# Performance work log

Hardware: AMD Instinct MI355X
Metric: run time of the kernel (lower is better)

## Reference

```python
import jax, jax.numpy as jnp
import numpy as np

EMBED_DIM = 512
N_HEADS = 8
HEAD_DIM = EMBED_DIM // N_HEADS
MAX_H = 64
MAX_W = 48
B, H, W = 2, 64, 48


def setup_inputs() -> dict:
    key = jax.random.key(0)
    k1, k2, k3, k4, k5 = jax.random.split(key, 5)
    x = jax.random.normal(k1, (B, H, W, EMBED_DIM), dtype=jnp.float32)
    # Linear weights stored as [in, out] (torch stores [out, in]; math is x @ W_in_out)
    w_qkv = jax.random.normal(k2, (EMBED_DIM, 3 * EMBED_DIM), dtype=jnp.float32) * (EMBED_DIM ** -0.5)
    w_out = jax.random.normal(k3, (EMBED_DIM, EMBED_DIM), dtype=jnp.float32) * (EMBED_DIM ** -0.5)
    rel_row_tab = jax.random.normal(k4, (2 * MAX_H - 1, N_HEADS), dtype=jnp.float32) * 0.02
    rel_col_tab = jax.random.normal(k5, (2 * MAX_W - 1, N_HEADS), dtype=jnp.float32) * 0.02
    return {"x": x, "w_qkv": w_qkv, "w_out": w_out,
            "rel_row_tab": rel_row_tab, "rel_col_tab": rel_col_tab}


def _rel_bias(rel_row_tab, rel_col_tab, height, width):
    # 2D relative position bias: [n_heads, S, S]
    row_idx = jnp.repeat(jnp.arange(height), width)          # [S]
    col_idx = jnp.tile(jnp.arange(width), height)            # [S]
    rel_row = jnp.clip(row_idx[:, None] - row_idx[None, :] + MAX_H - 1, 0, 2 * MAX_H - 2)
    rel_col = jnp.clip(col_idx[:, None] - col_idx[None, :] + MAX_W - 1, 0, 2 * MAX_W - 2)
    bias = rel_row_tab[rel_row] + rel_col_tab[rel_col]       # [S, S, n_heads]
    return jnp.transpose(bias, (2, 0, 1))                    # [n_heads, S, S]


def reference(x, w_qkv, w_out, rel_row_tab, rel_col_tab):
    b, h, w, d = x.shape
    s = h * w
    x_flat = x.reshape(b, s, d)
    qkv = x_flat @ w_qkv                                     # [b, s, 3d]
    qkv = qkv.reshape(b, s, 3, N_HEADS, HEAD_DIM)
    qkv = jnp.transpose(qkv, (2, 0, 3, 1, 4))                # [3, b, nh, s, hd]
    q, k, v = qkv[0], qkv[1], qkv[2]
    scale = HEAD_DIM ** -0.5
    attn = jnp.einsum('bhqd,bhkd->bhqk', q, k) * scale       # [b, nh, s, s]
    attn = attn + _rel_bias(rel_row_tab, rel_col_tab, h, w)[None]
    attn = jax.nn.softmax(attn, axis=-1)
    out = jnp.einsum('bhqk,bhkd->bhqd', attn, v)             # [b, nh, s, hd]
    out = jnp.transpose(out, (0, 2, 1, 3)).reshape(b, s, d)
    out = out @ w_out
    return out.reshape(b, h, w, d)
```

## Files before the change

### kernel.cpp

```cpp
#include <hip/hip_runtime.h>
#include <hip/hip_bf16.h>

#define S_TOK 3072
#define NHEADS 8

typedef __attribute__((ext_vector_type(8))) short short8;
typedef __attribute__((ext_vector_type(4))) float floatx4;
typedef __attribute__((ext_vector_type(4))) unsigned short ushortx4;

__device__ __forceinline__ unsigned short f2bf(float f) {
  union { float f; unsigned u; } v; v.f = f;
  unsigned r = v.u + 0x7fffu + ((v.u >> 16) & 1u);
  return (unsigned short)(r >> 16);
}
__device__ __forceinline__ float bf2f(unsigned short h) {
  union { unsigned u; float f; } v; v.u = (unsigned)h << 16;
  return v.f;
}
__device__ __forceinline__ unsigned pack2bf(float a, float b) {
  __hip_bfloat162 h = __float22bfloat162_rn(make_float2(a, b));
  union { __hip_bfloat162 h; unsigned u; } c; c.h = h;
  return c.u;
}
__device__ __forceinline__ void gload16(const void* g, void* l) {
  __builtin_amdgcn_global_load_lds(
      (const __attribute__((address_space(1))) unsigned int*)g,
      (__attribute__((address_space(3))) unsigned int*)l, 16, 0, 0);
}

__global__ __launch_bounds__(256) void ga_conv_x(
    const float* __restrict__ X, unsigned short* __restrict__ xh,
    unsigned short* __restrict__ xl) {
  const int c = blockIdx.x * 256 + threadIdx.x;
  const int m = c >> 6;
  const int c8 = (c & 63) << 3;
  const float* src = X + (size_t)m * 512 + c8;
  float4 v0 = *(const float4*)src, v1 = *(const float4*)(src + 4);
  float vv[8] = {v0.x, v0.y, v0.z, v0.w, v1.x, v1.y, v1.z, v1.w};
  union { unsigned short s[8]; short8 v; } hh, ll;
#pragma unroll
  for (int e = 0; e < 8; ++e) {
    hh.s[e] = f2bf(vv[e]);
    ll.s[e] = f2bf(vv[e] - bf2f(hh.s[e]));
  }
  const size_t dst = (size_t)m * 512 + (c8 ^ ((m & 7) << 3));
  *(short8*)&xh[dst] = hh.v;
  *(short8*)&xl[dst] = ll.v;
}

__global__ __launch_bounds__(256) void ga_conv_wt(
    const float* __restrict__ W, unsigned short* __restrict__ th,
    unsigned short* __restrict__ tl, int N) {
  const int k0 = blockIdx.x * 64, n0 = blockIdx.y * 64;
  const int t = threadIdx.x;
  __shared__ float Ts[64][65];
#pragma unroll
  for (int i = 0; i < 4; ++i) {
    const int r = (t >> 4) + i * 16, c4 = (t & 15) * 4;
    float4 v = *(const float4*)&W[(size_t)(k0 + r) * N + n0 + c4];
    Ts[r][c4] = v.x; Ts[r][c4 + 1] = v.y; Ts[r][c4 + 2] = v.z; Ts[r][c4 + 3] = v.w;
  }
  __syncthreads();
#pragma unroll
  for (int j = 0; j < 2; ++j) {
    const int chunk = t * 2 + j;
    const int nl = chunk >> 3, m8 = chunk & 7;
    const int n = n0 + nl;
    const int ks = (m8 * 8) ^ ((n & 7) << 3);
    union { unsigned short s[8]; short8 v; } hh, ll;
#pragma unroll
    for (int e = 0; e < 8; ++e) {
      float f = Ts[ks + e][nl];
      hh.s[e] = f2bf(f);
      ll.s[e] = f2bf(f - bf2f(hh.s[e]));
    }
    const size_t dst = (size_t)n * 512 + k0 + m8 * 8;
    *(short8*)&th[dst] = hh.v;
    *(short8*)&tl[dst] = ll.v;
  }
}

template <int BM, int BN, int WHICH>
__global__ __launch_bounds__(256, 2) void ga_mm3(
    const unsigned short* __restrict__ Ah, const unsigned short* __restrict__ Al,
    const unsigned short* __restrict__ Bh, const unsigned short* __restrict__ Bl,
    unsigned short* __restrict__ Qd, unsigned short* __restrict__ Kd,
    unsigned short* __restrict__ Vd, float* __restrict__ Out) {
  const int tid = threadIdx.x;
  const int w = tid >> 6, l = tid & 63;
  const int g = l >> 4, ln = l & 15;
  const int wm = w >> 1, wn = w & 1;
  const int m0 = blockIdx.x * BM;
  const int n0 = blockIdx.y * BN;
  constexpr int MI = BM / 32;
  constexpr int NI = BN / 32;
  __shared__ unsigned short Alds[2][BM * 64];
  __shared__ unsigned short Blds[2][BN * 64];
  floatx4 acc[MI][NI];
#pragma unroll
  for (int mi = 0; mi < MI; ++mi)
#pragma unroll
    for (int ni = 0; ni < NI; ++ni)
#pragma unroll
      for (int r = 0; r < 4; ++r) acc[mi][ni][r] = 0.f;

  for (int k0 = 0; k0 < 512; k0 += 64) {
    __syncthreads();
    {
      constexpr int PWA = (BM * 128) / 4096;
      constexpr int PWB = (BN * 128) / 4096;
      const char* ga_h = (const char*)(Ah + (size_t)m0 * 512 + k0);
      const char* ga_l = (const char*)(Al + (size_t)m0 * 512 + k0);
      const char* gb_h = (const char*)(Bh + (size_t)n0 * 512 + k0);
      const char* gb_l = (const char*)(Bl + (size_t)n0 * 512 + k0);
#pragma unroll
      for (int i = 0; i < PWA; ++i) {
        const int off = (w * PWA + i) * 1024;
        const int gb = ((off >> 7) + (l >> 3)) * 1024 + (l & 7) * 16;
        gload16(ga_h + gb, (char*)&Alds[0][0] + off);
        gload16(ga_l + gb, (char*)&Alds[1][0] + off);
      }
#pragma unroll
      for (int i = 0; i < PWB; ++i) {
        const int off = (w * PWB + i) * 1024;
        const int gb = ((off >> 7) + (l >> 3)) * 1024 + (l & 7) * 16;
        gload16(gb_h + gb, (char*)&Blds[0][0] + off);
        gload16(gb_l + gb, (char*)&Blds[1][0] + off);
      }
    }
    asm volatile("s_waitcnt vmcnt(0)" ::: "memory");
    __syncthreads();
#pragma unroll
    for (int kk = 0; kk < 64; kk += 32) {
      const int kbase = kk + g * 8;
      short8 ah[MI], al[MI], bh[NI], bl[NI];
#pragma unroll
      for (int mi = 0; mi < MI; ++mi) {
        const int row = wm * (BM / 2) + mi * 16 + ln;
        const int a = row * 64 + (kbase ^ ((row & 7) << 3));
        ah[mi] = *(const short8*)&Alds[0][a];
        al[mi] = *(const short8*)&Alds[1][a];
      }
#pragma unroll
      for (int ni = 0; ni < NI; ++ni) {
        const int row = wn * (BN / 2) + ni * 16 + ln;
        const int a = row * 64 + (kbase ^ ((row & 7) << 3));
        bh[ni] = *(const short8*)&Blds[0][a];
        bl[ni] = *(const short8*)&Blds[1][a];
      }
#pragma unroll
      for (int mi = 0; mi < MI; ++mi)
#pragma unroll
        for (int ni = 0; ni < NI; ++ni) {
          acc[mi][ni] = __builtin_amdgcn_mfma_f32_16x16x32_bf16(
              ah[mi], bh[ni], acc[mi][ni], 0, 0, 0);
          acc[mi][ni] = __builtin_amdgcn_mfma_f32_16x16x32_bf16(
              al[mi], bh[ni], acc[mi][ni], 0, 0, 0);
          acc[mi][ni] = __builtin_amdgcn_mfma_f32_16x16x32_bf16(
              ah[mi], bl[ni], acc[mi][ni], 0, 0, 0);
        }
    }
  }
  if constexpr (WHICH == 0) {
    const int b = m0 / S_TOK;
    const int s_base = (m0 % S_TOK) + wm * (BM / 2);
#pragma unroll
    for (int ni = 0; ni < NI; ++ni) {
      const int ng = n0 + wn * (BN / 2) + ni * 16;
      const int which = ng >> 9;
      const int h = (ng >> 6) & 7;
      const int d = (ng & 63) + ln;
      unsigned short* hp = (which == 0 ? Qd : which == 1 ? Kd : Vd) +
                           (size_t)(b * 8 + h) * S_TOK * 64;
      const float qs = (which == 0) ? 0.18033688f : 1.0f;
#pragma unroll
      for (int mi = 0; mi < MI; ++mi)
#pragma unroll
        for (int r = 0; r < 4; ++r) {
          const int s = s_base + mi * 16 + g * 4 + r;
          const size_t idx =
              (size_t)s * 64 + ((which == 1) ? (d ^ ((s & 7) << 3)) : d);
          hp[idx] = f2bf(acc[mi][ni][r] * qs);
        }
    }
  } else {
#pragma unroll
    for (int mi = 0; mi < MI; ++mi)
#pragma unroll
      for (int ni = 0; ni < NI; ++ni)
#pragma unroll
        for (int r = 0; r < 4; ++r)
          Out[(size_t)(m0 + wm * (BM / 2) + mi * 16 + g * 4 + r) * 512 + n0 +
              wn * (BN / 2) + ni * 16 + ln] = acc[mi][ni][r];
  }
}

__global__ __launch_bounds__(256) void ga_vtrans(
    const unsigned short* __restrict__ V, unsigned short* __restrict__ Vt2) {
  const int t = threadIdx.x;
  const int tile = blockIdx.x;
  const int bh = blockIdx.y;
  __shared__ unsigned short Ts[96][72];
  const unsigned short* vp = V + ((size_t)bh * S_TOK + tile * 96) * 64;
#pragma unroll
  for (int it = 0; it < 3; ++it) {
    int c = it * 256 + t;
    int s = c >> 3, d8 = c & 7;
    short8 v = *(const short8*)&vp[(size_t)s * 64 + d8 * 8];
    *(short8*)&Ts[s][d8 * 8] = v;
  }
  __syncthreads();
  unsigned short* op = Vt2 + ((size_t)bh * 32 + tile) * 8192;
#pragma unroll
  for (int it = 0; it < 4; ++it) {
    int c2 = it * 256 + t;
    int a = c2 * 8;
    int d = a >> 7;
    int pos0 = (a & 127) ^ ((d & 7) << 3);
    short8 o;
    if (pos0 < 96) {
      const int base = (pos0 & 96) + ((pos0 >> 3) & 3) * 4;
#pragma unroll
      for (int j = 0; j < 8; ++j) {
        const int key = base + ((j >> 2) << 4) + (j & 3);
        o[j] = (short)Ts[key][d];
      }
    } else {
#pragma unroll
      for (int j = 0; j < 8; ++j) o[j] = 0;
    }
    *(short8*)&op[a] = o;
  }
}

__global__ __launch_bounds__(256) void ga_attn16(
    const unsigned short* __restrict__ Q, const unsigned short* __restrict__ Kg,
    const unsigned short* __restrict__ Vt2, const float* __restrict__ rowtab,
    const float* __restrict__ coltab, float* __restrict__ Opart,
    float* __restrict__ Lpart, int tiles_per_split) {
  const int tid = threadIdx.x;
  const int w = tid >> 6;
  const int l = tid & 63;
  const int g = l >> 4;
  const int ln = l & 15;
  const int bh = blockIdx.y;
  const int sp = blockIdx.z;
  const int h = bh & 7;
  const int q0 = blockIdx.x * 128 + w * 32;

  __shared__ float rtab[127];
  __shared__ float ctab[95];
  __shared__ unsigned short Klds[6144];
  __shared__ unsigned short Vlds[8192];
  for (int i = tid; i < 127; i += 256) rtab[i] = rowtab[i * 8 + h] * 1.44269504f;
  for (int i = tid; i < 95; i += 256) ctab[i] = coltab[i * 8 + h] * 1.44269504f;
  __syncthreads();

  const unsigned short* Qp = Q + (size_t)bh * S_TOK * 64;
  const unsigned short* Kp = Kg + (size_t)bh * S_TOK * 64;
  const unsigned short* Vp = Vt2 + (size_t)bh * 32 * 8192;

  int qr[2], qc[2];
  short8 qf[2][2];
  float ctr[2][3][4];
#pragma unroll
  for (int u = 0; u < 2; ++u) {
    const int q = q0 + u * 16 + ln;
    qr[u] = q / 48;
    qc[u] = q - qr[u] * 48;
    qf[u][0] = *(const short8*)&Qp[(size_t)q * 64 + g * 8];
    qf[u][1] = *(const short8*)&Qp[(size_t)q * 64 + 32 + g * 8];
    const float* cb = &ctab[qc[u] - g * 4 + 47];
#pragma unroll
    for (int m = 0; m < 3; ++m)
#pragma unroll
      for (int r = 0; r < 4; ++r) ctr[u][m][r] = cb[-(16 * m + r)];
  }

  short8 ones;
  {
    union { unsigned short s[8]; short8 v; } on;
#pragma unroll
    for (int j = 0; j < 8; ++j) on.s[j] = 0x3F80;
    ones = on.v;
  }

  floatx4 o_acc[2][4];
  floatx4 o5[2];
#pragma unroll
  for (int u = 0; u < 2; ++u) {
#pragma unroll
    for (int r = 0; r < 4; ++r) o5[u][r] = 0.f;
#pragma unroll
    for (int dt = 0; dt < 4; ++dt)
#pragma unroll
      for (int r = 0; r < 4; ++r) o_acc[u][dt][r] = 0.f;
  }

  const int t0 = sp * tiles_per_split;
  for (int t = t0; t < t0 + tiles_per_split; ++t) {
    __syncthreads();
    {
      const char* kg = (const char*)(Kp + (size_t)t * 96 * 64);
      const char* vg = (const char*)(Vp + (size_t)t * 8192);
#pragma unroll
      for (int i = 0; i < 3; ++i) {
        const int off = w * 3072 + i * 1024;
        gload16(kg + off + l * 16, (char*)Klds + off);
      }
#pragma unroll
      for (int i = 0; i < 4; ++i) {
        const int off = w * 4096 + i * 1024;
        gload16(vg + off + l * 16, (char*)Vlds + off);
      }
      asm volatile("s_waitcnt vmcnt(0)" ::: "memory");
      __syncthreads();
    }
    float rt[2][2];
#pragma unroll
    for (int u = 0; u < 2; ++u) {
      rt[u][0] = rtab[qr[u] + 63 - 2 * t] - 12.0f;
      rt[u][1] = rtab[qr[u] + 62 - 2 * t] - 12.0f;
    }
    const int swz = (ln & 7) << 3;
#pragma unroll
    for (int kc32 = 0; kc32 < 3; ++kc32) {
      float e[2][2][4];
#pragma unroll
      for (int kh = 0; kh < 2; ++kh) {
        const int kt = kc32 * 2 + kh;
        const int rb = (kt * 16 + ln) * 64;
        short8 kf0 = *(const short8*)&Klds[rb + ((g * 8) ^ swz)];
        short8 kf1 = *(const short8*)&Klds[rb + ((32 + g * 8) ^ swz)];
        const int m = kt % 3, wrap = kt / 3;
#pragma unroll
        for (int u = 0; u < 2; ++u) {
          floatx4 s = {0.f, 0.f, 0.f, 0.f};
          s = __builtin_amdgcn_mfma_f32_16x16x32_bf16(kf0, qf[u][0], s, 0, 0, 0);
          s = __builtin_amdgcn_mfma_f32_16x16x32_bf16(kf1, qf[u][1], s, 0, 0, 0);
          const float rtw = rt[u][wrap];
#pragma unroll
          for (int r = 0; r < 4; ++r)
            e[u][kh][r] = __builtin_amdgcn_exp2f(s[r] + rtw + ctr[u][m][r]);
        }
      }
      short8 pf[2];
#pragma unroll
      for (int u = 0; u < 2; ++u) {
        union { unsigned uu[4]; short8 v; } pk;
        pk.uu[0] = pack2bf(e[u][0][0], e[u][0][1]);
        pk.uu[1] = pack2bf(e[u][0][2], e[u][0][3]);
        pk.uu[2] = pack2bf(e[u][1][0], e[u][1][1]);
        pk.uu[3] = pack2bf(e[u][1][2], e[u][1][3]);
        pf[u] = pk.v;
      }
#pragma unroll
      for (int dt = 0; dt < 4; ++dt) {
        const int vrow = dt * 16 + ln;
        short8 vf = *(const short8*)&Vlds[vrow * 128 +
                                          ((kc32 * 32 + g * 8) ^ swz)];
        o_acc[0][dt] =
            __builtin_amdgcn_mfma_f32_16x16x32_bf16(pf[0], vf, o_acc[0][dt], 0, 0, 0);
        o_acc[1][dt] =
            __builtin_amdgcn_mfma_f32_16x16x32_bf16(pf[1], vf, o_acc[1][dt], 0, 0, 0);
      }
      o5[0] = __builtin_amdgcn_mfma_f32_16x16x32_bf16(pf[0], ones, o5[0], 0, 0, 0);
      o5[1] = __builtin_amdgcn_mfma_f32_16x16x32_bf16(pf[1], ones, o5[1], 0, 0, 0);
    }
  }
  const size_t rowbase = (size_t)(sp * 16 + bh) * S_TOK;
#pragma unroll
  for (int u = 0; u < 2; ++u) {
    if (ln == 0) {
#pragma unroll
      for (int r = 0; r < 4; ++r)
        Lpart[rowbase + q0 + u * 16 + g * 4 + r] = o5[u][r];
    }
#pragma unroll
    for (int dt = 0; dt < 4; ++dt)
#pragma unroll
      for (int r = 0; r < 4; ++r)
        Opart[(rowbase + q0 + u * 16 + g * 4 + r) * 64 + dt * 16 + ln] =
            o_acc[u][dt][r];
  }
}

template <int NS>
__global__ __launch_bounds__(256) void ga_combine(
    const float* __restrict__ Opart, const float* __restrict__ Lpart,
    unsigned short* __restrict__ ch, unsigned short* __restrict__ cl) {
  const int c = blockIdx.x * 256 + threadIdx.x;
  const int m = c >> 6;
  const int col8 = (c & 63) << 3;
  const int b = (m >= S_TOK) ? 1 : 0;
  const int q = m - b * S_TOK;
  const int h = col8 >> 6, d0 = col8 & 63;
  const int bh = b * 8 + h;
  float v[8] = {0.f, 0.f, 0.f, 0.f, 0.f, 0.f, 0.f, 0.f};
  float ls = 0.f;
#pragma unroll
  for (int s = 0; s < NS; ++s) {
    const size_t row = (size_t)(s * 16 + bh) * S_TOK + q;
    ls += Lpart[row];
    const float4 o0 = *(const float4*)&Opart[row * 64 + d0];
    const float4 o1 = *(const float4*)&Opart[row * 64 + d0 + 4];
    v[0] += o0.x; v[1] += o0.y; v[2] += o0.z; v[3] += o0.w;
    v[4] += o1.x; v[5] += o1.y; v[6] += o1.z; v[7] += o1.w;
  }
  const float inv = 1.0f / ls;
  union { unsigned short s[8]; short8 vv; } hh, ll;
#pragma unroll
  for (int e = 0; e < 8; ++e) {
    float f = v[e] * inv;
    hh.s[e] = f2bf(f);
    ll.s[e] = f2bf(f - bf2f(hh.s[e]));
  }
  const size_t dst = (size_t)m * 512 + (col8 ^ ((m & 7) << 3));
  *(short8*)&ch[dst] = hh.vv;
  *(short8*)&cl[dst] = ll.vv;
}

extern "C" void kernel_launch(void* const* d_in, const int* in_sizes, int n_in,
                              void* d_out, int out_size, void* d_ws,
                              size_t ws_size, hipStream_t stream) {
  const float* x = (const float*)d_in[0];
  const float* w_qkv = (const float*)d_in[1];
  const float* w_out = (const float*)d_in[2];
  const float* rrow = (const float*)d_in[3];
  const float* rcol = (const float*)d_in[4];
  float* out = (float*)d_out;

  unsigned short* ws16 = (unsigned short*)d_ws;
  unsigned short* xh = ws16;
  unsigned short* xl = xh + 3145728;
  unsigned short* wqh = xl + 3145728;
  unsigned short* wql = wqh + 786432;
  unsigned short* woh = wql + 786432;
  unsigned short* wol = woh + 262144;
  unsigned short* Qb = wol + 262144;
  unsigned short* Kb = Qb + 3145728;
  unsigned short* Vb = Kb + 3145728;
  unsigned short* Vt2 = Vb + 3145728;
  float* Opart = (float*)(Vt2 + 4194304);
  const size_t base_bytes = (size_t)22020096 * 2;
  const size_t per_split = (size_t)(3145728 + 49152) * 4;
  int nsplit = (ws_size >= base_bytes + 2 * per_split) ? 2 : 1;
  float* Lpart = Opart + (size_t)nsplit * 3145728;

  ga_conv_x<<<1536, 256, 0, stream>>>(x, xh, xl);
  ga_conv_wt<<<dim3(8, 24), 256, 0, stream>>>(w_qkv, wqh, wql, 1536);
  ga_conv_wt<<<dim3(8, 8), 256, 0, stream>>>(w_out, woh, wol, 512);
  ga_mm3<128, 128, 0><<<dim3(48, 12), 256, 0, stream>>>(
      xh, xl, wqh, wql, Qb, Kb, Vb, nullptr);
  ga_vtrans<<<dim3(32, 16), 256, 0, stream>>>(Vb, Vt2);
  ga_attn16<<<dim3(24, 16, nsplit), 256, 0, stream>>>(
      Qb, Kb, Vt2, rrow, rcol, Opart, Lpart, 32 / nsplit);
  if (nsplit == 2)
    ga_combine<2><<<1536, 256, 0, stream>>>(Opart, Lpart, xh, xl);
  else
    ga_combine<1><<<1536, 256, 0, stream>>>(Opart, Lpart, xh, xl);
  ga_mm3<64, 64, 1><<<dim3(96, 8), 256, 0, stream>>>(
      xh, xl, woh, wol, nullptr, nullptr, nullptr, out);
}
```

Baseline: 137.0 us.

## Prefetch next K/V tile via registers in attention, remap blocks, fuse conversions

The attention kernel no longer loads each K/V tile directly into LDS and waits on it. It now prefetches the next tile into registers while computing on the current one, then writes those registers to LDS after a barrier. This hides global load latency, at the cost of extra VGPRs and a register-to-LDS copy. The grid is flattened and remapped so that consecutive workgroups spread across (b,h) pairs, likely to improve L2/XCD locality, and the three fp32-to-bf16 split conversion kernels are merged into a single launch.

```diff
diff --git a/kernel.cpp b/kernel.cpp
--- a/kernel.cpp
+++ b/kernel.cpp
@@ -28,31 +28,39 @@
       (__attribute__((address_space(3))) unsigned int*)l, 16, 0, 0);
 }
 
-__global__ __launch_bounds__(256) void ga_conv_x(
-    const float* __restrict__ X, unsigned short* __restrict__ xh,
-    unsigned short* __restrict__ xl) {
-  const int c = blockIdx.x * 256 + threadIdx.x;
-  const int m = c >> 6;
-  const int c8 = (c & 63) << 3;
-  const float* src = X + (size_t)m * 512 + c8;
-  float4 v0 = *(const float4*)src, v1 = *(const float4*)(src + 4);
-  float vv[8] = {v0.x, v0.y, v0.z, v0.w, v1.x, v1.y, v1.z, v1.w};
-  union { unsigned short s[8]; short8 v; } hh, ll;
-#pragma unroll
-  for (int e = 0; e < 8; ++e) {
-    hh.s[e] = f2bf(vv[e]);
-    ll.s[e] = f2bf(vv[e] - bf2f(hh.s[e]));
-  }
-  const size_t dst = (size_t)m * 512 + (c8 ^ ((m & 7) << 3));
-  *(short8*)&xh[dst] = hh.v;
-  *(short8*)&xl[dst] = ll.v;
-}
-
-__global__ __launch_bounds__(256) void ga_conv_wt(
-    const float* __restrict__ W, unsigned short* __restrict__ th,
-    unsigned short* __restrict__ tl, int N) {
-  const int k0 = blockIdx.x * 64, n0 = blockIdx.y * 64;
+__global__ __launch_bounds__(256) void ga_conv_all(
+    const float* __restrict__ X, const float* __restrict__ Wq,
+    const float* __restrict__ Wo, unsigned short* __restrict__ xh,
+    unsigned short* __restrict__ xl, unsigned short* __restrict__ wqh,
+    unsigned short* __restrict__ wql, unsigned short* __restrict__ woh,
+    unsigned short* __restrict__ wol) {
+  const int blk = blockIdx.x;
   const int t = threadIdx.x;
+  if (blk < 1536) {
+    const int c = blk * 256 + t;
+    const int m = c >> 6;
+    const int c8 = (c & 63) << 3;
+    const float* src = X + (size_t)m * 512 + c8;
+    float4 v0 = *(const float4*)src, v1 = *(const float4*)(src + 4);
+    float vv[8] = {v0.x, v0.y, v0.z, v0.w, v1.x, v1.y, v1.z, v1.w};
+    union { unsigned short s[8]; short8 v; } hh, ll;
+#pragma unroll
+    for (int e = 0; e < 8; ++e) {
+      hh.s[e] = f2bf(vv[e]);
+      ll.s[e] = f2bf(vv[e] - bf2f(hh.s[e]));
+    }
+    const size_t dst = (size_t)m * 512 + (c8 ^ ((m & 7) << 3));
+    *(short8*)&xh[dst] = hh.v;
+    *(short8*)&xl[dst] = ll.v;
+    return;
+  }
+  const int wq = (blk < 1728);
+  const int b2 = wq ? (blk - 1536) : (blk - 1728);
+  const int N = wq ? 1536 : 512;
+  const float* W = wq ? Wq : Wo;
+  unsigned short* th = wq ? wqh : woh;
+  unsigned short* tl = wq ? wql : wol;
+  const int k0 = (b2 & 7) * 64, n0 = (b2 >> 3) * 64;
   __shared__ float Ts[64][65];
 #pragma unroll
   for (int i = 0; i < 4; ++i) {
@@ -237,16 +245,22 @@
     const unsigned short* __restrict__ Q, const unsigned short* __restrict__ Kg,
     const unsigned short* __restrict__ Vt2, const float* __restrict__ rowtab,
     const float* __restrict__ coltab, float* __restrict__ Opart,
-    float* __restrict__ Lpart, int tiles_per_split) {
+    float* __restrict__ Lpart, int nsplit) {
   const int tid = threadIdx.x;
   const int w = tid >> 6;
   const int l = tid & 63;
   const int g = l >> 4;
   const int ln = l & 15;
-  const int bh = blockIdx.y;
-  const int sp = blockIdx.z;
+  const int wgid = blockIdx.x;
+  const int idx = wgid >> 3;
+  const int bpb = 24 * nsplit;
+  const int bh = ((wgid & 7) << 1) + idx / bpb;
+  const int rem = idx % bpb;
+  const int sp = rem / 24;
+  const int qb = rem % 24;
   const int h = bh & 7;
-  const int q0 = blockIdx.x * 128 + w * 32;
+  const int q0 = qb * 128 + w * 32;
+  const int tiles_per_split = 32 / nsplit;
 
   __shared__ float rtab[127];
   __shared__ float ctab[95];
@@ -254,7 +268,6 @@
   __shared__ unsigned short Vlds[8192];
   for (int i = tid; i < 127; i += 256) rtab[i] = rowtab[i * 8 + h] * 1.44269504f;
   for (int i = tid; i < 95; i += 256) ctab[i] = coltab[i * 8 + h] * 1.44269504f;
-  __syncthreads();
 
   const unsigned short* Qp = Q + (size_t)bh * S_TOK * 64;
   const unsigned short* Kp = Kg + (size_t)bh * S_TOK * 64;
@@ -263,6 +276,21 @@
   int qr[2], qc[2];
   short8 qf[2][2];
   float ctr[2][3][4];
+  uint4 kreg[3], vreg[4];
+
+  const int t0 = sp * tiles_per_split;
+  const int tend = t0 + tiles_per_split;
+  {
+    const char* kg = (const char*)(Kp + (size_t)t0 * 96 * 64);
+    const char* vg = (const char*)(Vp + (size_t)t0 * 8192);
+#pragma unroll
+    for (int i = 0; i < 3; ++i)
+      kreg[i] = *(const uint4*)(kg + w * 3072 + i * 1024 + l * 16);
+#pragma unroll
+    for (int i = 0; i < 4; ++i)
+      vreg[i] = *(const uint4*)(vg + w * 4096 + i * 1024 + l * 16);
+  }
+  __syncthreads();
 #pragma unroll
   for (int u = 0; u < 2; ++u) {
     const int q = q0 + u * 16 + ln;
@@ -276,6 +304,13 @@
 #pragma unroll
       for (int r = 0; r < 4; ++r) ctr[u][m][r] = cb[-(16 * m + r)];
   }
+#pragma unroll
+  for (int i = 0; i < 3; ++i)
+    *(uint4*)((char*)Klds + w * 3072 + i * 1024 + l * 16) = kreg[i];
+#pragma unroll
+  for (int i = 0; i < 4; ++i)
+    *(uint4*)((char*)Vlds + w * 4096 + i * 1024 + l * 16) = vreg[i];
+  __syncthreads();
 
   short8 ones;
   {
@@ -297,24 +332,17 @@
       for (int r = 0; r < 4; ++r) o_acc[u][dt][r] = 0.f;
   }
 
-  const int t0 = sp * tiles_per_split;
-  for (int t = t0; t < t0 + tiles_per_split; ++t) {
-    __syncthreads();
-    {
-      const char* kg = (const char*)(Kp + (size_t)t * 96 * 64);
-      const char* vg = (const char*)(Vp + (size_t)t * 8192);
-#pragma unroll
-      for (int i = 0; i < 3; ++i) {
-        const int off = w * 3072 + i * 1024;
-        gload16(kg + off + l * 16, (char*)Klds + off);
-      }
-#pragma unroll
-      for (int i = 0; i < 4; ++i) {
-        const int off = w * 4096 + i * 1024;
-        gload16(vg + off + l * 16, (char*)Vlds + off);
-      }
-      asm volatile("s_waitcnt vmcnt(0)" ::: "memory");
-      __syncthreads();
+  for (int t = t0; t < tend; ++t) {
+    const bool pf = (t + 1 < tend);
+    if (pf) {
+      const char* kg = (const char*)(Kp + (size_t)(t + 1) * 96 * 64);
+      const char* vg = (const char*)(Vp + (size_t)(t + 1) * 8192);
+#pragma unroll
+      for (int i = 0; i < 3; ++i)
+        kreg[i] = *(const uint4*)(kg + w * 3072 + i * 1024 + l * 16);
+#pragma unroll
+      for (int i = 0; i < 4; ++i)
+        vreg[i] = *(const uint4*)(vg + w * 4096 + i * 1024 + l * 16);
     }
     float rt[2][2];
 #pragma unroll
@@ -344,7 +372,7 @@
             e[u][kh][r] = __builtin_amdgcn_exp2f(s[r] + rtw + ctr[u][m][r]);
         }
       }
-      short8 pf[2];
+      short8 pf2[2];
 #pragma unroll
       for (int u = 0; u < 2; ++u) {
         union { unsigned uu[4]; short8 v; } pk;
@@ -352,7 +380,7 @@
         pk.uu[1] = pack2bf(e[u][0][2], e[u][0][3]);
         pk.uu[2] = pack2bf(e[u][1][0], e[u][1][1]);
         pk.uu[3] = pack2bf(e[u][1][2], e[u][1][3]);
-        pf[u] = pk.v;
+        pf2[u] = pk.v;
       }
 #pragma unroll
       for (int dt = 0; dt < 4; ++dt) {
@@ -360,12 +388,22 @@
         short8 vf = *(const short8*)&Vlds[vrow * 128 +
                                           ((kc32 * 32 + g * 8) ^ swz)];
         o_acc[0][dt] =
-            __builtin_amdgcn_mfma_f32_16x16x32_bf16(pf[0], vf, o_acc[0][dt], 0, 0, 0);
+            __builtin_amdgcn_mfma_f32_16x16x32_bf16(pf2[0], vf, o_acc[0][dt], 0, 0, 0);
         o_acc[1][dt] =
-            __builtin_amdgcn_mfma_f32_16x16x32_bf16(pf[1], vf, o_acc[1][dt], 0, 0, 0);
-      }
-      o5[0] = __builtin_amdgcn_mfma_f32_16x16x32_bf16(pf[0], ones, o5[0], 0, 0, 0);
-      o5[1] = __builtin_amdgcn_mfma_f32_16x16x32_bf16(pf[1], ones, o5[1], 0, 0, 0);
+            __builtin_amdgcn_mfma_f32_16x16x32_bf16(pf2[1], vf, o_acc[1][dt], 0, 0, 0);
+      }
+      o5[0] = __builtin_amdgcn_mfma_f32_16x16x32_bf16(pf2[0], ones, o5[0], 0, 0, 0);
+      o5[1] = __builtin_amdgcn_mfma_f32_16x16x32_bf16(pf2[1], ones, o5[1], 0, 0, 0);
+    }
+    __syncthreads();
+    if (pf) {
+#pragma unroll
+      for (int i = 0; i < 3; ++i)
+        *(uint4*)((char*)Klds + w * 3072 + i * 1024 + l * 16) = kreg[i];
+#pragma unroll
+      for (int i = 0; i < 4; ++i)
+        *(uint4*)((char*)Vlds + w * 4096 + i * 1024 + l * 16) = vreg[i];
+      __syncthreads();
     }
   }
   const size_t rowbase = (size_t)(sp * 16 + bh) * S_TOK;
@@ -447,14 +485,13 @@
   int nsplit = (ws_size >= base_bytes + 2 * per_split) ? 2 : 1;
   float* Lpart = Opart + (size_t)nsplit * 3145728;
 
-  ga_conv_x<<<1536, 256, 0, stream>>>(x, xh, xl);
-  ga_conv_wt<<<dim3(8, 24), 256, 0, stream>>>(w_qkv, wqh, wql, 1536);
-  ga_conv_wt<<<dim3(8, 8), 256, 0, stream>>>(w_out, woh, wol, 512);
+  ga_conv_all<<<1792, 256, 0, stream>>>(x, w_qkv, w_out, xh, xl, wqh, wql, woh,
+                                        wol);
   ga_mm3<128, 128, 0><<<dim3(48, 12), 256, 0, stream>>>(
       xh, xl, wqh, wql, Qb, Kb, Vb, nullptr);
   ga_vtrans<<<dim3(32, 16), 256, 0, stream>>>(Vb, Vt2);
-  ga_attn16<<<dim3(24, 16, nsplit), 256, 0, stream>>>(
-      Qb, Kb, Vt2, rrow, rcol, Opart, Lpart, 32 / nsplit);
+  ga_attn16<<<24 * 16 * nsplit, 256, 0, stream>>>(
+      Qb, Kb, Vt2, rrow, rcol, Opart, Lpart, nsplit);
   if (nsplit == 2)
     ga_combine<2><<<1536, 256, 0, stream>>>(Opart, Lpart, xh, xl);
   else
```

Result: slower. 197.4 us (+44.0%).
